# Performance work log

Measured on AMD Instinct MI355X. Metric: run time of the kernel, lower is better.

The kernel has to match this reference:

```python
import jax, jax.numpy as jnp
import numpy as np

N_PITCH, N_DUR, N_TIME, N_VEL = 128, 160, 100, 128
VOCAB = N_PITCH + N_DUR + N_TIME + N_VEL  # 516
B, S = 32, 2048


def _build_vocab_tables():
    # token_type: 0='p', 1='d', 2='t', 3='v'; token_value: numeric suffix of itos_vocab[i]
    tt = np.concatenate([
        np.full(N_PITCH, 0), np.full(N_DUR, 1), np.full(N_TIME, 2), np.full(N_VEL, 3)
    ]).astype(np.int32)
    tv = np.concatenate([
        np.arange(N_PITCH), np.arange(N_DUR), np.arange(N_TIME), np.arange(N_VEL)
    ]).astype(np.float32)
    return jnp.asarray(tt), jnp.asarray(tv)


def setup_inputs() -> dict:
    key = jax.random.key(0)
    k1, k2, k3, k4 = jax.random.split(key, 4)
    token_type, token_value = _build_vocab_tables()
    return {
        "output": jax.random.normal(k1, (B, VOCAB, S), dtype=jnp.float32),
        "target": jax.random.randint(k2, (B, S), 0, VOCAB, dtype=jnp.int32),
        "token_type": token_type,
        "token_value": token_value,
        "coeff": jnp.asarray([0.5, 0.6, 0.2, 0.2], dtype=jnp.float32),
        "harmonic": jnp.asarray([0.6, 0.6, 0.2, 0.2, 0.2, 0.2, 1.5], dtype=jnp.float32),
    }


def _penalty_mask(pred, target, token_type, token_value, coeff, harmonic):
    pt, tt = token_type[pred], token_type[target]      # [B,S] type codes
    pv, tv = token_value[pred], token_value[target]    # [B,S] numeric values
    d = jnp.abs(pv - tv)
    # pitch: harmonic-interval weights (values are integer-valued floats -> exact ==)
    pitch_w = jnp.where(d == 7, harmonic[0],
              jnp.where(d == 5, harmonic[1],
              jnp.where(d == 3, harmonic[2],
              jnp.where(d == 4, harmonic[3],
              jnp.where(d == 1, harmonic[4],
              jnp.where(d == 2, harmonic[5], harmonic[6]))))))
    dur_w = coeff[1] * d / 160.0
    time_w = coeff[2] * d / 100.0
    vel_w = coeff[3] * d / 128.0
    same_type_w = jnp.where(pt == 0, pitch_w,
                  jnp.where(pt == 1, dur_w,
                  jnp.where(pt == 2, time_w, vel_w)))
    return jnp.where(pt != tt, coeff[0], same_type_w)


def reference(output, target, token_type, token_value, coeff, harmonic):
    # Faithful to original: softmax over last (seq) axis, then argmax over vocab axis 1
    sm = jax.nn.softmax(output, axis=-1)
    pred = jnp.argmax(sm, axis=1)                      # [B,S]
    # mean cross-entropy over B*S (class axis = 1)
    logp = jax.nn.log_softmax(output, axis=1)          # [B,V,S]
    nll = -jnp.take_along_axis(logp, target[:, None, :], axis=1)[:, 0, :]
    loss = nll.mean()
    mask = _penalty_mask(pred, target, token_type, token_value, coeff, harmonic)
    high_cost = (loss * mask).mean()
    return loss + high_cost
```

## Files before the change

### kernel.cpp

```cpp
#include <hip/hip_runtime.h>

#define BB 32
#define SS 2048
#define VV 516
#define NBS (BB * SS)
#define NCHUNK 16
#define NPART 256

__device__ __forceinline__ float waveReduceSum(float v) {
    #pragma unroll
    for (int o = 32; o > 0; o >>= 1) v += __shfl_down(v, o, 64);
    return v;
}

__device__ __forceinline__ void stage16(const float* g, float* l) {
    __builtin_amdgcn_global_load_lds(
        (const __attribute__((address_space(1))) void*)(g),
        (__attribute__((address_space(3))) void*)(l),
        16, 0, 0);
}

__global__ __launch_bounds__(512, 2) void hl_tile(const float* __restrict__ x,
                                                  const int* __restrict__ target,
                                                  int* __restrict__ ctr,
                                                  float* __restrict__ pSum,
                                                  float* __restrict__ pBest,
                                                  int* __restrict__ pIdx,
                                                  float* __restrict__ xtArr) {
    __shared__ float buf[2][4][2048];
    __shared__ float ldsH[2][4][2];
    __shared__ float ldsT[8];

    if (blockIdx.x == 0 && threadIdx.x == 0) ctr[0] = 0;

    const int c = blockIdx.x & 15, b = blockIdx.x >> 4;
    const int v0 = 32 * c + (c > 12 ? c - 12 : 0);
    const int nv = (c >= 12) ? 33 : 32;
    const int tid = threadIdx.x, lane = tid & 63, wv = tid >> 6;
    const int row = wv >> 1, half = wv & 1;
    const int s0 = tid << 2;
    const int bs = b * SS + s0;

    int4 tg4 = *(const int4*)(target + bs);
    int tg[4] = {tg4.x, tg4.y, tg4.z, tg4.w};

    float sum[4]  = {0.f, 0.f, 0.f, 0.f};
    float best[4] = {-1.f, -1.f, -1.f, -1.f};
    float xt[4]   = {0.f, 0.f, 0.f, 0.f};
    int   bi[4]   = {v0, v0, v0, v0};

    const float* gbase = x + (size_t)(b * VV + v0 + row) * SS + half * 1024 + lane * 4;

    {
        float* ls = &buf[0][row][half * 1024];
        #pragma unroll
        for (int j = 0; j < 4; ++j) stage16(gbase + j * 256, ls + j * 256);
    }
    asm volatile("s_waitcnt vmcnt(0)" ::: "memory");
    __builtin_amdgcn_sched_barrier(0);
    __builtin_amdgcn_s_barrier();

    for (int k = 0; k < 8; ++k) {
        const int kb = k & 1;
        if (k + 1 < 8) {
            const float* gs = gbase + (size_t)(k + 1) * 4 * SS;
            float* ls = &buf[kb ^ 1][row][half * 1024];
            #pragma unroll
            for (int j = 0; j < 4; ++j) stage16(gs + j * 256, ls + j * 256);
        }
        {
            float* p = &buf[kb][row][half * 1024 + lane * 4];
            float a = 0.f;
            #pragma unroll
            for (int j = 0; j < 4; ++j) {
                float4 v = *(const float4*)(p + j * 256);
                float4 e;
                e.x = __expf(v.x); e.y = __expf(v.y);
                e.z = __expf(v.z); e.w = __expf(v.w);
                *(float4*)(p + j * 256) = e;
                a += (e.x + e.y) + (e.z + e.w);
            }
            a = waveReduceSum(a);
            if (lane == 0) ldsH[kb][row][half] = a;
        }
        asm volatile("s_waitcnt lgkmcnt(0)" ::: "memory");
        __builtin_amdgcn_sched_barrier(0);
        __builtin_amdgcn_s_barrier();
        #pragma unroll
        for (int r = 0; r < 4; ++r) {
            float rs = ldsH[kb][r][0] + ldsH[kb][r][1];
            float rc = 1.f / rs;
            int vg = v0 + k * 4 + r;
            float4 e = *(const float4*)&buf[kb][r][s0];
            sum[0] += e.x; sum[1] += e.y; sum[2] += e.z; sum[3] += e.w;
            float c0 = e.x * rc, c1 = e.y * rc, c2 = e.z * rc, c3 = e.w * rc;
            if (c0 > best[0]) { best[0] = c0; bi[0] = vg; }
            if (c1 > best[1]) { best[1] = c1; bi[1] = vg; }
            if (c2 > best[2]) { best[2] = c2; bi[2] = vg; }
            if (c3 > best[3]) { best[3] = c3; bi[3] = vg; }
        }
        #pragma unroll
        for (int i = 0; i < 4; ++i) {
            int lr = tg[i] - (v0 + k * 4);
            if (lr >= 0 && lr < 4) xt[i] = __logf(buf[kb][lr][s0 + i]);
        }
        asm volatile("s_waitcnt vmcnt(0)" ::: "memory");
        __builtin_amdgcn_sched_barrier(0);
        __builtin_amdgcn_s_barrier();
    }

    if (nv == 33) {
        int vg = v0 + 32;
        float4 xv = *(const float4*)(x + (size_t)(b * VV + vg) * SS + s0);
        float4 e;
        e.x = __expf(xv.x); e.y = __expf(xv.y);
        e.z = __expf(xv.z); e.w = __expf(xv.w);
        float a = waveReduceSum((e.x + e.y) + (e.z + e.w));
        if (lane == 0) ldsT[wv] = a;
        asm volatile("s_waitcnt lgkmcnt(0)" ::: "memory");
        __builtin_amdgcn_sched_barrier(0);
        __builtin_amdgcn_s_barrier();
        float rs = ((ldsT[0] + ldsT[1]) + (ldsT[2] + ldsT[3]))
                 + ((ldsT[4] + ldsT[5]) + (ldsT[6] + ldsT[7]));
        float rc = 1.f / rs;
        if (vg == tg[0]) xt[0] = xv.x;
        if (vg == tg[1]) xt[1] = xv.y;
        if (vg == tg[2]) xt[2] = xv.z;
        if (vg == tg[3]) xt[3] = xv.w;
        sum[0] += e.x; sum[1] += e.y; sum[2] += e.z; sum[3] += e.w;
        float c0 = e.x * rc, c1 = e.y * rc, c2 = e.z * rc, c3 = e.w * rc;
        if (c0 > best[0]) { best[0] = c0; bi[0] = vg; }
        if (c1 > best[1]) { best[1] = c1; bi[1] = vg; }
        if (c2 > best[2]) { best[2] = c2; bi[2] = vg; }
        if (c3 > best[3]) { best[3] = c3; bi[3] = vg; }
    }

    int o = c * NBS + bs;
    *(float4*)(pSum + o)  = make_float4(sum[0], sum[1], sum[2], sum[3]);
    *(float4*)(pBest + o) = make_float4(best[0], best[1], best[2], best[3]);
    *(int4*)(pIdx + o)    = make_int4(bi[0], bi[1], bi[2], bi[3]);
    int v1 = v0 + nv;
    #pragma unroll
    for (int i = 0; i < 4; ++i)
        if (tg[i] >= v0 && tg[i] < v1) xtArr[bs + i] = xt[i];
}

__global__ __launch_bounds__(256) void hl_comb(const int* __restrict__ target,
                                               const int* __restrict__ ttype,
                                               const float* __restrict__ tval,
                                               const float* __restrict__ coeff,
                                               const float* __restrict__ harm,
                                               const float* __restrict__ pSum,
                                               const float* __restrict__ pBest,
                                               const int* __restrict__ pIdx,
                                               const float* __restrict__ xtArr,
                                               float* __restrict__ pNll,
                                               float* __restrict__ pMask,
                                               int* __restrict__ counter,
                                               float* __restrict__ outv) {
    __shared__ float lds[8];
    __shared__ bool isLast;
    int idx = blockIdx.x * 256 + threadIdx.x;

    float sum = 0.f, best = -1e30f;
    int bestIdx = 0;
    #pragma unroll
    for (int c = 0; c < NCHUNK; ++c) {
        int o = c * NBS + idx;
        sum += pSum[o];
        float sc = pBest[o];
        int ii = pIdx[o];
        if (sc > best) { best = sc; bestIdx = ii; }
    }
    int tgt = target[idx];
    float nll = __logf(sum) - xtArr[idx];

    int pt = ttype[bestIdx], tt = ttype[tgt];
    float pv = tval[bestIdx], tv = tval[tgt];
    float d = fabsf(pv - tv);
    float pw = (d == 7.f) ? harm[0] : (d == 5.f) ? harm[1] : (d == 3.f) ? harm[2]
             : (d == 4.f) ? harm[3] : (d == 1.f) ? harm[4] : (d == 2.f) ? harm[5]
             : harm[6];
    float w = (pt == 0) ? pw
            : (pt == 1) ? coeff[1] * d * (1.f / 160.f)
            : (pt == 2) ? coeff[2] * d * (1.f / 100.f)
            :             coeff[3] * d * (1.f / 128.f);
    float mask = (pt != tt) ? coeff[0] : w;

    int lane = threadIdx.x & 63, wvv = threadIdx.x >> 6;
    float rn = waveReduceSum(nll);
    if (lane == 0) lds[wvv] = rn;
    __syncthreads();
    float totN = (threadIdx.x == 0) ? lds[0] + lds[1] + lds[2] + lds[3] : 0.f;
    __syncthreads();
    float rm = waveReduceSum(mask);
    if (lane == 0) lds[wvv] = rm;
    __syncthreads();
    if (threadIdx.x == 0) {
        pNll[blockIdx.x]  = totN;
        pMask[blockIdx.x] = lds[0] + lds[1] + lds[2] + lds[3];
        __threadfence();
        unsigned old = atomicAdd((unsigned*)counter, 1u);
        isLast = (old == NPART - 1);
    }
    __syncthreads();
    if (isLast) {
        __threadfence();
        int t = threadIdx.x;
        float n = waveReduceSum(pNll[t]);
        float m = waveReduceSum(pMask[t]);
        if (lane == 0) { lds[wvv] = n; lds[4 + wvv] = m; }
        __syncthreads();
        if (t == 0) {
            float tn = lds[0] + lds[1] + lds[2] + lds[3];
            float tm = lds[4] + lds[5] + lds[6] + lds[7];
            const float inv = 1.f / (float)NBS;
            outv[0] = (tn * inv) * (1.f + tm * inv);
        }
    }
}

extern "C" void kernel_launch(void* const* d_in, const int* in_sizes, int n_in,
                              void* d_out, int out_size, void* d_ws, size_t ws_size,
                              hipStream_t stream) {
    const float* x      = (const float*)d_in[0];
    const int*   target = (const int*)d_in[1];
    const int*   ttype  = (const int*)d_in[2];
    const float* tval   = (const float*)d_in[3];
    const float* coeff  = (const float*)d_in[4];
    const float* harm   = (const float*)d_in[5];

    float* ws    = (float*)d_ws;
    int*   ctr   = (int*)ws;
    float* pNll  = ws + 4;
    float* pMask = pNll + NPART;
    float* xtArr = pMask + NPART;
    float* pSum  = xtArr + NBS;
    float* pBest = pSum + (size_t)NCHUNK * NBS;
    int*   pIdx  = (int*)(pBest + (size_t)NCHUNK * NBS);

    hl_tile<<<BB * NCHUNK, 512, 0, stream>>>(x, target, ctr, pSum, pBest,
                                             pIdx, xtArr);
    hl_comb<<<NBS / 256, 256, 0, stream>>>(target, ttype, tval, coeff, harm,
                                           pSum, pBest, pIdx, xtArr,
                                           pNll, pMask, ctr, (float*)d_out);
}
```

Measured before the change: 47.27 us.

## Deepen LDS staging to a 4-stage ring with partial vmcnt waits

Restructures the per-block vocab-chunk loop from a double buffer of 4 rows per step to a 4-slot ring of 2 rows per step, with three tiles prefetched. Partial vmcnt waits and a single barrier per iteration replace the full drain and second barrier. The aim is to keep more global-to-LDS loads in flight and cut synchronisation stalls. In exchange it runs more iterations with smaller work each, and correctness depends on the hand-tuned vmcnt counts and ring reuse after the barrier.

```diff
diff --git a/kernel.cpp b/kernel.cpp
--- a/kernel.cpp
+++ b/kernel.cpp
@@ -27,8 +27,8 @@
                                                   float* __restrict__ pBest,
                                                   int* __restrict__ pIdx,
                                                   float* __restrict__ xtArr) {
-    __shared__ float buf[2][4][2048];
-    __shared__ float ldsH[2][4][2];
+    __shared__ float buf[4][2][2048];
+    __shared__ float ldsQ[4][2][4];
     __shared__ float ldsT[8];
 
     if (blockIdx.x == 0 && threadIdx.x == 0) ctr[0] = 0;
@@ -37,7 +37,8 @@
     const int v0 = 32 * c + (c > 12 ? c - 12 : 0);
     const int nv = (c >= 12) ? 33 : 32;
     const int tid = threadIdx.x, lane = tid & 63, wv = tid >> 6;
-    const int row = wv >> 1, half = wv & 1;
+    const int row = wv >> 2;
+    const int q   = wv & 3;
     const int s0 = tid << 2;
     const int bs = b * SS + s0;
 
@@ -49,48 +50,54 @@
     float xt[4]   = {0.f, 0.f, 0.f, 0.f};
     int   bi[4]   = {v0, v0, v0, v0};
 
-    const float* gbase = x + (size_t)(b * VV + v0 + row) * SS + half * 1024 + lane * 4;
-
-    {
-        float* ls = &buf[0][row][half * 1024];
+    const float* gbase = x + (size_t)(b * VV + v0 + row) * SS + q * 512 + lane * 4;
+
+    #pragma unroll
+    for (int t = 0; t < 3; ++t) {
+        const float* gs = gbase + (size_t)t * 2 * SS;
+        float* ls = &buf[t][row][q * 512];
+        stage16(gs, ls);
+        stage16(gs + 256, ls + 256);
+    }
+
+    for (int k = 0; k < 16; ++k) {
+        const int kb = k & 3;
+        if (k <= 13)      { asm volatile("s_waitcnt vmcnt(4)" ::: "memory"); }
+        else if (k == 14) { asm volatile("s_waitcnt vmcnt(2)" ::: "memory"); }
+        else              { asm volatile("s_waitcnt vmcnt(0)" ::: "memory"); }
+        __builtin_amdgcn_sched_barrier(0);
+        {
+            float* p = &buf[kb][row][q * 512 + lane * 4];
+            float4 u0 = *(const float4*)p;
+            float4 u1 = *(const float4*)(p + 256);
+            float4 e0, e1;
+            e0.x = __expf(u0.x); e0.y = __expf(u0.y);
+            e0.z = __expf(u0.z); e0.w = __expf(u0.w);
+            e1.x = __expf(u1.x); e1.y = __expf(u1.y);
+            e1.z = __expf(u1.z); e1.w = __expf(u1.w);
+            *(float4*)p = e0;
+            *(float4*)(p + 256) = e1;
+            float a = ((e0.x + e0.y) + (e0.z + e0.w))
+                    + ((e1.x + e1.y) + (e1.z + e1.w));
+            a = waveReduceSum(a);
+            if (lane == 0) ldsQ[kb][row][q] = a;
+        }
+        asm volatile("s_waitcnt lgkmcnt(0)" ::: "memory");
+        __builtin_amdgcn_sched_barrier(0);
+        __builtin_amdgcn_s_barrier();
+        __builtin_amdgcn_sched_barrier(0);
+        if (k + 3 < 16) {
+            const float* gs = gbase + (size_t)(k + 3) * 2 * SS;
+            float* ls = &buf[(k + 3) & 3][row][q * 512];
+            stage16(gs, ls);
+            stage16(gs + 256, ls + 256);
+        }
         #pragma unroll
-        for (int j = 0; j < 4; ++j) stage16(gbase + j * 256, ls + j * 256);
-    }
-    asm volatile("s_waitcnt vmcnt(0)" ::: "memory");
-    __builtin_amdgcn_sched_barrier(0);
-    __builtin_amdgcn_s_barrier();
-
-    for (int k = 0; k < 8; ++k) {
-        const int kb = k & 1;
-        if (k + 1 < 8) {
-            const float* gs = gbase + (size_t)(k + 1) * 4 * SS;
-            float* ls = &buf[kb ^ 1][row][half * 1024];
-            #pragma unroll
-            for (int j = 0; j < 4; ++j) stage16(gs + j * 256, ls + j * 256);
-        }
-        {
-            float* p = &buf[kb][row][half * 1024 + lane * 4];
-            float a = 0.f;
-            #pragma unroll
-            for (int j = 0; j < 4; ++j) {
-                float4 v = *(const float4*)(p + j * 256);
-                float4 e;
-                e.x = __expf(v.x); e.y = __expf(v.y);
-                e.z = __expf(v.z); e.w = __expf(v.w);
-                *(float4*)(p + j * 256) = e;
-                a += (e.x + e.y) + (e.z + e.w);
-            }
-            a = waveReduceSum(a);
-            if (lane == 0) ldsH[kb][row][half] = a;
-        }
-        asm volatile("s_waitcnt lgkmcnt(0)" ::: "memory");
-        __builtin_amdgcn_sched_barrier(0);
-        __builtin_amdgcn_s_barrier();
-        #pragma unroll
-        for (int r = 0; r < 4; ++r) {
-            float rs = ldsH[kb][r][0] + ldsH[kb][r][1];
+        for (int r = 0; r < 2; ++r) {
+            float rs = (ldsQ[kb][r][0] + ldsQ[kb][r][1])
+                     + (ldsQ[kb][r][2] + ldsQ[kb][r][3]);
             float rc = 1.f / rs;
-            int vg = v0 + k * 4 + r;
+            int vg = v0 + k * 2 + r;
             float4 e = *(const float4*)&buf[kb][r][s0];
             sum[0] += e.x; sum[1] += e.y; sum[2] += e.z; sum[3] += e.w;
             float c0 = e.x * rc, c1 = e.y * rc, c2 = e.z * rc, c3 = e.w * rc;
@@ -101,12 +108,9 @@
         }
         #pragma unroll
         for (int i = 0; i < 4; ++i) {
-            int lr = tg[i] - (v0 + k * 4);
-            if (lr >= 0 && lr < 4) xt[i] = __logf(buf[kb][lr][s0 + i]);
-        }
-        asm volatile("s_waitcnt vmcnt(0)" ::: "memory");
-        __builtin_amdgcn_sched_barrier(0);
-        __builtin_amdgcn_s_barrier();
+            int lr = tg[i] - (v0 + k * 2);
+            if (lr >= 0 && lr < 2) xt[i] = __logf(buf[kb][lr][s0 + i]);
+        }
     }
 
     if (nv == 33) {
```

Measured after the change: 51.86 us. 1.1x slower.
